# Kernel tuning notes

Hardware: AMD Instinct MI355X
Metric: run time of the kernel (lower is better)

The kernel has to match this reference:

```python
import jax, jax.numpy as jnp
import numpy as np

N, E, B, H, L = 50000, 800000, 256, 128, 4
AF, EF, GF, T = 108, 41, 239, 5
EPS = 1e-5


def _ln(x, g, b):
    m = jnp.mean(x, -1, keepdims=True)
    v = jnp.var(x, -1, keepdims=True)
    return (x - m) * jax.lax.rsqrt(v + EPS) * g + b


def setup_inputs() -> dict:
    key = jax.random.key(0)
    ks = jax.random.split(key, 20)
    w = lambda k, s: jax.random.normal(k, s, jnp.float32) * 0.05
    return {
        "x": jax.random.normal(ks[0], (N, AF), jnp.float32),
        "edge_attr": jax.random.normal(ks[1], (E, EF), jnp.float32),
        "global_features": jax.random.normal(ks[2], (B, GF), jnp.float32),
        "ae_w1": w(ks[3], (AF, H)), "ae_b1": jnp.zeros((H,), jnp.float32),
        "ae_w2": w(ks[4], (H, H)), "ae_b2": jnp.zeros((H,), jnp.float32),
        "ew1": w(ks[5], (L, EF, H)), "eb1": jnp.zeros((L, H), jnp.float32),
        "ew2": w(ks[6], (L, H, H)), "eb2": jnp.zeros((L, H), jnp.float32),
        "nw1": w(ks[7], (L, H, H)), "nb1": jnp.zeros((L, H), jnp.float32),
        "nw2": w(ks[8], (L, H, H)), "nb2": jnp.zeros((L, H), jnp.float32),
        "ln_g": jnp.ones((L, H), jnp.float32), "ln_b": jnp.zeros((L, H), jnp.float32),
        "gw": w(ks[9], (GF, H)), "gb": jnp.zeros((H,), jnp.float32),
        "ow1": w(ks[10], (2 * H, H)), "ob1": jnp.zeros((H,), jnp.float32),
        "ow2": w(ks[11], (H, H // 2)), "ob2": jnp.zeros((H // 2,), jnp.float32),
        "ow3": w(ks[12], (H // 2, T)), "ob3": jnp.zeros((T,), jnp.float32),
        "edge_index": jax.random.randint(ks[13], (2, E), 0, N, jnp.int32),
        "batch": jnp.sort(jax.random.randint(ks[14], (N,), 0, B, jnp.int32)),
    }


def reference(x, edge_attr, global_features, ae_w1, ae_b1, ae_w2, ae_b2,
              ew1, eb1, ew2, eb2, nw1, nb1, nw2, nb2, ln_g, ln_b,
              gw, gb, ow1, ob1, ow2, ob2, ow3, ob3, edge_index, batch):
    silu = jax.nn.silu
    # atom embedding
    h = silu(x @ ae_w1 + ae_b1) @ ae_w2 + ae_b2  # [N,H]
    src, dst = edge_index[0], edge_index[1]
    for l in range(L):
        # continuous-filter: edge MLP -> gather x_j -> multiply -> scatter-add
        Wf = silu(edge_attr @ ew1[l] + eb1[l]) @ ew2[l] + eb2[l]  # [E,H]
        msg = h[src] * Wf                                          # [E,H]
        agg = jax.ops.segment_sum(msg, dst, num_segments=N)        # [N,H]
        out = silu(agg @ nw1[l] + nb1[l]) @ nw2[l] + nb2[l]
        h = _ln(h + out, ln_g[l], ln_b[l])
    # global mean pool over graphs
    counts = jnp.clip(jax.ops.segment_sum(jnp.ones((N,), jnp.float32), batch, num_segments=B), 1.0)
    graph = jax.ops.segment_sum(h, batch, num_segments=B) / counts[:, None]  # [B,H]
    gp = silu(global_features @ gw + gb)                                      # [B,H]
    comb = jnp.concatenate([graph, gp], axis=-1)                              # [B,2H]
    hid = silu(silu(comb @ ow1 + ob1) @ ow2 + ob2)  # dropout is identity in eval
    return hid @ ow3 + ob3                           # [B,T]
```

## Files before the change

### kernel.cpp

```cpp
#include <hip/hip_runtime.h>
#include <math.h>

#define NATOM 50000
#define NEDGE 800000
#define NGRAPH 256
#define HD 128
#define NL 4
#define AFD 108
#define EFD 41
#define GFD 239
#define TOUT 5
#define LNEPS 1e-5f

typedef __attribute__((ext_vector_type(8))) short short8;
typedef __attribute__((ext_vector_type(4))) float f32x4;

__device__ __forceinline__ float silu_f(float v) {
    return v * __builtin_amdgcn_rcpf(1.f + __expf(-v));
}

__device__ __forceinline__ unsigned short f2b(float f) {
    union { float f; unsigned u; } x; x.f = f;
    unsigned r = x.u + 0x7fffu + ((x.u >> 16) & 1u);
    return (unsigned short)(r >> 16);
}

__global__ void hist_kernel(const int* __restrict__ dst, int* __restrict__ count) {
    for (int e = blockIdx.x * blockDim.x + threadIdx.x; e < NEDGE; e += gridDim.x * blockDim.x)
        atomicAdd(&count[dst[e]], 1);
}

__global__ void scan_kernel(const int* __restrict__ count, int* __restrict__ rowptr,
                            int* __restrict__ cursor) {
    __shared__ int s_w[4];
    __shared__ int s_carry;
    const int t = threadIdx.x, lane = t & 63, wv = t >> 6;
    if (t == 0) { s_carry = 0; rowptr[0] = 0; }
    __syncthreads();
    for (int base = 0; base < NATOM; base += 256) {
        int v = (base + t < NATOM) ? count[base + t] : 0;
        int x = v;
#pragma unroll
        for (int off = 1; off < 64; off <<= 1) {
            int y = __shfl_up(x, off);
            if (lane >= off) x += y;
        }
        if (lane == 63) s_w[wv] = x;
        __syncthreads();
        int wvoff = s_carry;
        for (int w = 0; w < wv; w++) wvoff += s_w[w];
        int incl = x + wvoff;
        if (base + t < NATOM) { rowptr[base + t + 1] = incl; cursor[base + t] = incl - v; }
        __syncthreads();
        if (t == 255) s_carry = incl;
        __syncthreads();
    }
}

__global__ void pos_kernel(const int* __restrict__ dst, const int* __restrict__ src,
                           int* __restrict__ cursor, int* __restrict__ pos,
                           int* __restrict__ ssrc) {
    for (int e = blockIdx.x * blockDim.x + threadIdx.x; e < NEDGE; e += gridDim.x * blockDim.x) {
        int d = dst[e];
        int p = atomicAdd(&cursor[d], 1);
        pos[e] = p;
        if (ssrc) ssrc[p] = src[e];
    }
}

__global__ void wconv_kernel(const float* __restrict__ ew1, const float* __restrict__ ew2,
                             unsigned short* __restrict__ w1t, unsigned short* __restrict__ w2t) {
    int idx = blockIdx.x * 256 + threadIdx.x;
    const int n1 = NL * HD * 64;
    if (idx < n1) {
        int l = idx / (HD * 64); int rem = idx - l * HD * 64; int n = rem >> 6; int k = rem & 63;
        float v = (k < EFD) ? ew1[((size_t)l * EFD + k) * HD + n] : 0.f;
        w1t[idx] = f2b(v);
    } else {
        int j = idx - n1;
        if (j < NL * HD * HD) {
            int l = j / (HD * HD); int rem = j - l * HD * HD; int n = rem >> 7; int k = rem & 127;
            w2t[j] = f2b(ew2[((size_t)l * HD + k) * HD + n]);
        }
    }
}

__global__ __launch_bounds__(256, 2) void atom_kernel(
    const float* __restrict__ x, const float* __restrict__ w1, const float* __restrict__ b1,
    const float* __restrict__ w2, const float* __restrict__ b2, float* __restrict__ h)
{
    __shared__ float s_x[64 * AFD];
    __shared__ float s_hid[64 * HD];
    const int t = threadIdx.x, cg = t & 31, rg = t >> 5, c4 = cg * 4;
    const int r0 = blockIdx.x * 64;

    for (int i = t; i < 64 * AFD; i += 256) {
        size_t g = (size_t)r0 * AFD + i;
        s_x[i] = (g < (size_t)NATOM * AFD) ? x[g] : 0.f;
    }
    float4 bb1 = *(const float4*)&b1[c4];
    float4 bb2 = *(const float4*)&b2[c4];
    __syncthreads();

    float4 acc[8];
#pragma unroll
    for (int i = 0; i < 8; i++) acc[i] = bb1;
    for (int k = 0; k < AFD; k++) {
        float4 w = *(const float4*)&w1[k * HD + c4];
#pragma unroll
        for (int i = 0; i < 8; i++) {
            float a = s_x[(rg * 8 + i) * AFD + k];
            acc[i].x += a * w.x; acc[i].y += a * w.y; acc[i].z += a * w.z; acc[i].w += a * w.w;
        }
    }
#pragma unroll
    for (int i = 0; i < 8; i++) {
        float4 v = acc[i];
        v.x = silu_f(v.x); v.y = silu_f(v.y); v.z = silu_f(v.z); v.w = silu_f(v.w);
        *(float4*)&s_hid[(rg * 8 + i) * HD + c4] = v;
    }
    __syncthreads();

    float4 o[8];
#pragma unroll
    for (int i = 0; i < 8; i++) o[i] = bb2;
    for (int j = 0; j < HD; j++) {
        float4 w = *(const float4*)&w2[j * HD + c4];
#pragma unroll
        for (int i = 0; i < 8; i++) {
            float a = s_hid[(rg * 8 + i) * HD + j];
            o[i].x += a * w.x; o[i].y += a * w.y; o[i].z += a * w.z; o[i].w += a * w.w;
        }
    }
#pragma unroll
    for (int i = 0; i < 8; i++) {
        int r = r0 + rg * 8 + i;
        if (r < NATOM) *(float4*)&h[(size_t)r * HD + c4] = o[i];
    }
}

__global__ __launch_bounds__(256) void wf_kernel(
    const float* __restrict__ edge_attr,
    const unsigned short* __restrict__ w1t, const float* __restrict__ b1,
    const unsigned short* __restrict__ w2t, const float* __restrict__ b2,
    const int* __restrict__ pos, float* __restrict__ wf)
{
    __shared__ __align__(16) unsigned short s_a1[64 * 64];
    __shared__ __align__(16) unsigned short s_hid[64 * 128];
    __shared__ __align__(16) float s_out[32 * 132];
    __shared__ int s_pos[64];

    const int t = threadIdx.x;
    const int wv = t >> 6, lane = t & 63;
    const int lr = lane & 15, lk = lane >> 4;

    short8 wb1[2][2], wb2[2][4];
    float b1v[2], b2v[2];
#pragma unroll
    for (int nt = 0; nt < 2; nt++) {
        int n = (wv * 2 + nt) * 16 + lr;
        b1v[nt] = b1[n]; b2v[nt] = b2[n];
#pragma unroll
        for (int kk = 0; kk < 2; kk++) wb1[nt][kk] = *(const short8*)&w1t[n * 64 + kk * 32 + lk * 8];
#pragma unroll
        for (int kk = 0; kk < 4; kk++) wb2[nt][kk] = *(const short8*)&w2t[n * 128 + kk * 32 + lk * 8];
    }

    int stg_byte[11];
    bool stg_ok[11];
#pragma unroll
    for (int j = 0; j < 11; j++) {
        int i = t + j * 256;
        stg_ok[j] = (i < 64 * EFD);
        int e = i / EFD, k = i - e * EFD;
        stg_byte[j] = e * 128 + ((2 * k) ^ ((e & 7) << 4));
    }

    for (int i = t; i < 64 * 64; i += 256) s_a1[i] = 0;
    __syncthreads();

    const int tc = t & 31, tr8 = t >> 5;
    const int ntiles = NEDGE / 64;
    for (int tile = blockIdx.x; tile < ntiles; tile += gridDim.x) {
        const int e0 = tile * 64;
        if (t < 64) s_pos[t] = pos[e0 + t];
        const float* ea = edge_attr + (size_t)e0 * EFD;
#pragma unroll
        for (int j = 0; j < 11; j++)
            if (stg_ok[j])
                *(unsigned short*)((char*)s_a1 + stg_byte[j]) = f2b(ea[t + j * 256]);
        __syncthreads();

        f32x4 acc1[4][2];
#pragma unroll
        for (int rt = 0; rt < 4; rt++) {
            int row = rt * 16 + lr;
            int sw = (row & 7) << 4;
            short8 a0 = *(const short8*)((const char*)s_a1 + row * 128 + ((lk * 16) ^ sw));
            short8 a1 = *(const short8*)((const char*)s_a1 + row * 128 + ((64 + lk * 16) ^ sw));
#pragma unroll
            for (int nt = 0; nt < 2; nt++) {
                f32x4 c = {0.f, 0.f, 0.f, 0.f};
                c = __builtin_amdgcn_mfma_f32_16x16x32_bf16(a0, wb1[nt][0], c, 0, 0, 0);
                c = __builtin_amdgcn_mfma_f32_16x16x32_bf16(a1, wb1[nt][1], c, 0, 0, 0);
                acc1[rt][nt] = c;
            }
        }
#pragma unroll
        for (int rt = 0; rt < 4; rt++) {
#pragma unroll
            for (int nt = 0; nt < 2; nt++) {
#pragma unroll
                for (int r = 0; r < 4; r++) {
                    int row = rt * 16 + lk * 4 + r;
                    int col = (wv * 2 + nt) * 16 + lr;
                    float v = silu_f(acc1[rt][nt][r] + b1v[nt]);
                    int byte = row * 256 + ((2 * col) ^ ((row & 7) << 4));
                    *(unsigned short*)((char*)s_hid + byte) = f2b(v);
                }
            }
        }
        __syncthreads();

        f32x4 acc2[4][2];
#pragma unroll
        for (int rt = 0; rt < 4; rt++) {
            int row = rt * 16 + lr;
            int sw = (row & 7) << 4;
            short8 ha[4];
#pragma unroll
            for (int kk = 0; kk < 4; kk++)
                ha[kk] = *(const short8*)((const char*)s_hid + row * 256 + ((kk * 64 + lk * 16) ^ sw));
#pragma unroll
            for (int nt = 0; nt < 2; nt++) {
                f32x4 c = {0.f, 0.f, 0.f, 0.f};
#pragma unroll
                for (int kk = 0; kk < 4; kk++)
                    c = __builtin_amdgcn_mfma_f32_16x16x32_bf16(ha[kk], wb2[nt][kk], c, 0, 0, 0);
                acc2[rt][nt] = c;
            }
        }

#pragma unroll
        for (int hf = 0; hf < 2; hf++) {
#pragma unroll
            for (int rr = 0; rr < 2; rr++) {
                int rt = hf * 2 + rr;
#pragma unroll
                for (int nt = 0; nt < 2; nt++)
#pragma unroll
                    for (int r = 0; r < 4; r++)
                        s_out[(rr * 16 + lk * 4 + r) * 132 + (wv * 2 + nt) * 16 + lr] =
                            silu_f(acc2[rt][nt][r] + b2v[nt]);
            }
            __syncthreads();
#pragma unroll
            for (int i = 0; i < 4; i++) {
                int lrow = tr8 * 4 + i;
                int p = s_pos[hf * 32 + lrow];
                *(float4*)&wf[(size_t)p * HD + tc * 4] = *(const float4*)&s_out[lrow * 132 + tc * 4];
            }
            __syncthreads();
        }
    }
}

__global__ void mul_kernel(const float* __restrict__ h, const int* __restrict__ src,
                           const int* __restrict__ pos, float* __restrict__ wf) {
    for (long long idx = (long long)blockIdx.x * 256 + threadIdx.x;
         idx < (long long)NEDGE * 32; idx += (long long)gridDim.x * 256) {
        int e = (int)(idx >> 5), q = (int)(idx & 31);
        int p = pos[e], s = src[e];
        float4 w = *(const float4*)&wf[(size_t)p * HD + q * 4];
        float4 hv = *(const float4*)&h[(size_t)s * HD + q * 4];
        w.x *= hv.x; w.y *= hv.y; w.z *= hv.z; w.w *= hv.w;
        *(float4*)&wf[(size_t)p * HD + q * 4] = w;
    }
}

template<bool GATHER>
__global__ __launch_bounds__(256, 2) void node_kernel(
    const float* __restrict__ wfm, const int* __restrict__ rowptr, const int* __restrict__ ssrc,
    const float* __restrict__ h_in,
    const float* __restrict__ w1, const float* __restrict__ b1,
    const float* __restrict__ w2, const float* __restrict__ b2,
    const float* __restrict__ lg, const float* __restrict__ lb,
    float* __restrict__ h_out)
{
    __shared__ float s_in[64 * HD];
    __shared__ float s_hid[64 * HD];
    __shared__ int s_rp[65];
    const int t = threadIdx.x, cg = t & 31, rg = t >> 5, c4 = cg * 4;
    const int r0 = blockIdx.x * 64;

    if (t < 65) {
        int idx = r0 + t;
        if (idx > NATOM) idx = NATOM;
        s_rp[t] = rowptr[idx];
    }
    float4 bb1 = *(const float4*)&b1[c4];
    float4 bb2 = *(const float4*)&b2[c4];
    float4 g4 = *(const float4*)&lg[c4];
    float4 lb4 = *(const float4*)&lb[c4];
    __syncthreads();

#pragma unroll
    for (int i = 0; i < 8; i++) {
        int rr = rg * 8 + i;
        int beg = s_rp[rr], end = s_rp[rr + 1];
        float4 a0 = make_float4(0.f, 0.f, 0.f, 0.f);
        float4 a1 = make_float4(0.f, 0.f, 0.f, 0.f);
        float4 a2 = make_float4(0.f, 0.f, 0.f, 0.f);
        float4 a3 = make_float4(0.f, 0.f, 0.f, 0.f);
        int p = beg;
        for (; p + 3 < end; p += 4) {
            float4 m0 = *(const float4*)&wfm[(size_t)(p + 0) * HD + c4];
            float4 m1 = *(const float4*)&wfm[(size_t)(p + 1) * HD + c4];
            float4 m2 = *(const float4*)&wfm[(size_t)(p + 2) * HD + c4];
            float4 m3 = *(const float4*)&wfm[(size_t)(p + 3) * HD + c4];
            if (GATHER) {
                int s0 = ssrc[p + 0], s1 = ssrc[p + 1], s2 = ssrc[p + 2], s3 = ssrc[p + 3];
                float4 h0 = *(const float4*)&h_in[(size_t)s0 * HD + c4];
                float4 h1 = *(const float4*)&h_in[(size_t)s1 * HD + c4];
                float4 h2 = *(const float4*)&h_in[(size_t)s2 * HD + c4];
                float4 h3 = *(const float4*)&h_in[(size_t)s3 * HD + c4];
                a0.x = fmaf(m0.x, h0.x, a0.x); a0.y = fmaf(m0.y, h0.y, a0.y);
                a0.z = fmaf(m0.z, h0.z, a0.z); a0.w = fmaf(m0.w, h0.w, a0.w);
                a1.x = fmaf(m1.x, h1.x, a1.x); a1.y = fmaf(m1.y, h1.y, a1.y);
                a1.z = fmaf(m1.z, h1.z, a1.z); a1.w = fmaf(m1.w, h1.w, a1.w);
                a2.x = fmaf(m2.x, h2.x, a2.x); a2.y = fmaf(m2.y, h2.y, a2.y);
                a2.z = fmaf(m2.z, h2.z, a2.z); a2.w = fmaf(m2.w, h2.w, a2.w);
                a3.x = fmaf(m3.x, h3.x, a3.x); a3.y = fmaf(m3.y, h3.y, a3.y);
                a3.z = fmaf(m3.z, h3.z, a3.z); a3.w = fmaf(m3.w, h3.w, a3.w);
            } else {
                a0.x += m0.x; a0.y += m0.y; a0.z += m0.z; a0.w += m0.w;
                a1.x += m1.x; a1.y += m1.y; a1.z += m1.z; a1.w += m1.w;
                a2.x += m2.x; a2.y += m2.y; a2.z += m2.z; a2.w += m2.w;
                a3.x += m3.x; a3.y += m3.y; a3.z += m3.z; a3.w += m3.w;
            }
        }
        for (; p < end; p++) {
            float4 m0 = *(const float4*)&wfm[(size_t)p * HD + c4];
            if (GATHER) {
                int s0 = ssrc[p];
                float4 h0 = *(const float4*)&h_in[(size_t)s0 * HD + c4];
                a0.x = fmaf(m0.x, h0.x, a0.x); a0.y = fmaf(m0.y, h0.y, a0.y);
                a0.z = fmaf(m0.z, h0.z, a0.z); a0.w = fmaf(m0.w, h0.w, a0.w);
            } else {
                a0.x += m0.x; a0.y += m0.y; a0.z += m0.z; a0.w += m0.w;
            }
        }
        a0.x += a1.x + a2.x + a3.x; a0.y += a1.y + a2.y + a3.y;
        a0.z += a1.z + a2.z + a3.z; a0.w += a1.w + a2.w + a3.w;
        *(float4*)&s_in[rr * HD + c4] = a0;
    }
    __syncthreads();

    float4 acc[8];
#pragma unroll
    for (int i = 0; i < 8; i++) acc[i] = bb1;
    for (int k = 0; k < HD; k++) {
        float4 w = *(const float4*)&w1[k * HD + c4];
#pragma unroll
        for (int i = 0; i < 8; i++) {
            float a = s_in[(rg * 8 + i) * HD + k];
            acc[i].x += a * w.x; acc[i].y += a * w.y; acc[i].z += a * w.z; acc[i].w += a * w.w;
        }
    }
#pragma unroll
    for (int i = 0; i < 8; i++) {
        float4 v = acc[i];
        v.x = silu_f(v.x); v.y = silu_f(v.y); v.z = silu_f(v.z); v.w = silu_f(v.w);
        *(float4*)&s_hid[(rg * 8 + i) * HD + c4] = v;
    }
    __syncthreads();

    float4 o[8];
#pragma unroll
    for (int i = 0; i < 8; i++) o[i] = bb2;
    for (int j = 0; j < HD; j++) {
        float4 w = *(const float4*)&w2[j * HD + c4];
#pragma unroll
        for (int i = 0; i < 8; i++) {
            float a = s_hid[(rg * 8 + i) * HD + j];
            o[i].x += a * w.x; o[i].y += a * w.y; o[i].z += a * w.z; o[i].w += a * w.w;
        }
    }
#pragma unroll
    for (int i = 0; i < 8; i++) {
        int r = r0 + rg * 8 + i;
        float4 hv = make_float4(0.f, 0.f, 0.f, 0.f);
        if (r < NATOM) hv = *(const float4*)&h_in[(size_t)r * HD + c4];
        float4 v;
        v.x = hv.x + o[i].x; v.y = hv.y + o[i].y; v.z = hv.z + o[i].z; v.w = hv.w + o[i].w;
        float s1 = v.x + v.y + v.z + v.w;
        float s2 = v.x * v.x + v.y * v.y + v.z * v.z + v.w * v.w;
#pragma unroll
        for (int off = 16; off >= 1; off >>= 1) {
            s1 += __shfl_xor(s1, off);
            s2 += __shfl_xor(s2, off);
        }
        float mean = s1 * (1.f / HD);
        float var = s2 * (1.f / HD) - mean * mean;
        float rstd = rsqrtf(var + LNEPS);
        float4 y;
        y.x = (v.x - mean) * rstd * g4.x + lb4.x;
        y.y = (v.y - mean) * rstd * g4.y + lb4.y;
        y.z = (v.z - mean) * rstd * g4.z + lb4.z;
        y.w = (v.w - mean) * rstd * g4.w + lb4.w;
        if (r < NATOM) *(float4*)&h_out[(size_t)r * HD + c4] = y;
    }
}

__global__ __launch_bounds__(128) void head_kernel(
    const float* __restrict__ h, const float* __restrict__ gfeat,
    const float* __restrict__ gw, const float* __restrict__ gb,
    const float* __restrict__ ow1, const float* __restrict__ ob1,
    const float* __restrict__ ow2, const float* __restrict__ ob2,
    const float* __restrict__ ow3, const float* __restrict__ ob3,
    const int* __restrict__ batch, float* __restrict__ out)
{
    __shared__ float comb[2 * HD];
    __shared__ float h1[HD];
    __shared__ float h2[64];
    const int b = blockIdx.x;
    const int c = threadIdx.x;

    int lo = 0, hi = NATOM;
    while (lo < hi) { int m = (lo + hi) >> 1; if (batch[m] < b) lo = m + 1; else hi = m; }
    const int start = lo;
    hi = NATOM;
    while (lo < hi) { int m = (lo + hi) >> 1; if (batch[m] < b + 1) lo = m + 1; else hi = m; }
    const int end = lo;

    float s = 0.f;
    for (int r = start; r < end; r++) s += h[(size_t)r * HD + c];
    float cnt = (float)(end - start);
    if (cnt < 1.f) cnt = 1.f;
    comb[c] = s / cnt;

    float a = gb[c];
    for (int k = 0; k < GFD; k++) a += gfeat[b * GFD + k] * gw[k * HD + c];
    comb[HD + c] = silu_f(a);
    __syncthreads();

    float u = ob1[c];
    for (int j = 0; j < 2 * HD; j++) u += comb[j] * ow1[j * HD + c];
    h1[c] = silu_f(u);
    __syncthreads();

    if (c < 64) {
        float v = ob2[c];
        for (int j = 0; j < HD; j++) v += h1[j] * ow2[j * 64 + c];
        h2[c] = silu_f(v);
    }
    __syncthreads();

    if (c < TOUT) {
        float v = ob3[c];
        for (int j = 0; j < 64; j++) v += h2[j] * ow3[j * TOUT + c];
        out[b * TOUT + c] = v;
    }
}

extern "C" void kernel_launch(void* const* d_in, const int* in_sizes, int n_in,
                              void* d_out, int out_size, void* d_ws, size_t ws_size,
                              hipStream_t stream) {
    const float* x        = (const float*)d_in[0];
    const float* edge_attr= (const float*)d_in[1];
    const float* gfeat    = (const float*)d_in[2];
    const float* ae_w1    = (const float*)d_in[3];
    const float* ae_b1    = (const float*)d_in[4];
    const float* ae_w2    = (const float*)d_in[5];
    const float* ae_b2    = (const float*)d_in[6];
    const float* ew1      = (const float*)d_in[7];
    const float* eb1      = (const float*)d_in[8];
    const float* ew2      = (const float*)d_in[9];
    const float* eb2      = (const float*)d_in[10];
    const float* nw1      = (const float*)d_in[11];
    const float* nb1      = (const float*)d_in[12];
    const float* nw2      = (const float*)d_in[13];
    const float* nb2      = (const float*)d_in[14];
    const float* ln_g     = (const float*)d_in[15];
    const float* ln_b     = (const float*)d_in[16];
    const float* gw       = (const float*)d_in[17];
    const float* gb       = (const float*)d_in[18];
    const float* ow1      = (const float*)d_in[19];
    const float* ob1      = (const float*)d_in[20];
    const float* ow2      = (const float*)d_in[21];
    const float* ob2      = (const float*)d_in[22];
    const float* ow3      = (const float*)d_in[23];
    const float* ob3      = (const float*)d_in[24];
    const int* edge_index = (const int*)d_in[25];
    const int* batch      = (const int*)d_in[26];

    const int* src = edge_index;
    const int* dst = edge_index + NEDGE;
    const int row_blocks = (NATOM + 63) / 64;

    float* h0 = (float*)d_ws;
    size_t fA = (size_t)NATOM * HD * 2 + (size_t)NEDGE * HD;
    size_t intsA = (size_t)NATOM * 3 + 4 + (size_t)NEDGE * 2;
    size_t wele = (size_t)NL * HD * 64 + (size_t)NL * HD * HD;
    size_t needA = fA * 4 + intsA * 4 + wele * 2;

    bool modeA = (ws_size >= needA);

    float* h1   = modeA ? (h0 + (size_t)NATOM * HD) : h0;
    float* wf   = (modeA ? h1 : h0) + (size_t)NATOM * HD;
    int* count  = (int*)(wf + (size_t)NEDGE * HD);
    int* rowptr = count + NATOM;
    int* cursor = rowptr + NATOM + 4;
    int* pos    = cursor + NATOM;
    int* ssrc   = modeA ? (pos + NEDGE) : nullptr;
    unsigned short* w1t = (unsigned short*)(modeA ? (ssrc + NEDGE) : (pos + NEDGE));
    unsigned short* w2t = w1t + NL * HD * 64;

    hipMemsetAsync(count, 0, NATOM * sizeof(int), stream);
    hist_kernel<<<1024, 256, 0, stream>>>(dst, count);
    scan_kernel<<<1, 256, 0, stream>>>(count, rowptr, cursor);
    pos_kernel<<<1024, 256, 0, stream>>>(dst, src, cursor, pos, ssrc);
    wconv_kernel<<<(NL * HD * 64 + NL * HD * HD + 255) / 256, 256, 0, stream>>>(ew1, ew2, w1t, w2t);

    atom_kernel<<<row_blocks, 256, 0, stream>>>(x, ae_w1, ae_b1, ae_w2, ae_b2, h0);

    const float* cur = h0;
    float* nxt = modeA ? h1 : h0;
    for (int l = 0; l < NL; l++) {
        wf_kernel<<<2048, 256, 0, stream>>>(
            edge_attr,
            w1t + (size_t)l * HD * 64, eb1 + (size_t)l * HD,
            w2t + (size_t)l * HD * HD, eb2 + (size_t)l * HD,
            pos, wf);
        if (modeA) {
            node_kernel<true><<<row_blocks, 256, 0, stream>>>(
                wf, rowptr, ssrc, cur,
                nw1 + (size_t)l * HD * HD, nb1 + (size_t)l * HD,
                nw2 + (size_t)l * HD * HD, nb2 + (size_t)l * HD,
                ln_g + (size_t)l * HD, ln_b + (size_t)l * HD,
                nxt);
            const float* tmp = cur; cur = nxt; nxt = (float*)tmp;
        } else {
            mul_kernel<<<2048, 256, 0, stream>>>(h0, src, pos, wf);
            node_kernel<false><<<row_blocks, 256, 0, stream>>>(
                wf, rowptr, nullptr, h0,
                nw1 + (size_t)l * HD * HD, nb1 + (size_t)l * HD,
                nw2 + (size_t)l * HD * HD, nb2 + (size_t)l * HD,
                ln_g + (size_t)l * HD, ln_b + (size_t)l * HD,
                h0);
        }
    }

    head_kernel<<<NGRAPH, 128, 0, stream>>>(
        cur, gfeat, gw, gb, ow1, ob1, ow2, ob2, ow3, ob3, batch, (float*)d_out);
}
```

Measured before the change: 2.208 ms.

## Widen scan, shrink LDS in wf and node kernels, unroll pooling sum

```diff
diff --git a/kernel.cpp b/kernel.cpp
--- a/kernel.cpp
+++ b/kernel.cpp
@@ -32,12 +32,12 @@
 
 __global__ void scan_kernel(const int* __restrict__ count, int* __restrict__ rowptr,
                             int* __restrict__ cursor) {
-    __shared__ int s_w[4];
+    __shared__ int s_w[16];
     __shared__ int s_carry;
     const int t = threadIdx.x, lane = t & 63, wv = t >> 6;
     if (t == 0) { s_carry = 0; rowptr[0] = 0; }
     __syncthreads();
-    for (int base = 0; base < NATOM; base += 256) {
+    for (int base = 0; base < NATOM; base += 1024) {
         int v = (base + t < NATOM) ? count[base + t] : 0;
         int x = v;
 #pragma unroll
@@ -52,7 +52,7 @@
         int incl = x + wvoff;
         if (base + t < NATOM) { rowptr[base + t + 1] = incl; cursor[base + t] = incl - v; }
         __syncthreads();
-        if (t == 255) s_carry = incl;
+        if (t == 1023) s_carry = incl;
         __syncthreads();
     }
 }
@@ -147,7 +147,7 @@
 {
     __shared__ __align__(16) unsigned short s_a1[64 * 64];
     __shared__ __align__(16) unsigned short s_hid[64 * 128];
-    __shared__ __align__(16) float s_out[32 * 132];
+    __shared__ __align__(16) float s_out[16 * 132];
     __shared__ int s_pos[64];
 
     const int t = threadIdx.x;
@@ -242,22 +242,18 @@
         }
 
 #pragma unroll
-        for (int hf = 0; hf < 2; hf++) {
-#pragma unroll
-            for (int rr = 0; rr < 2; rr++) {
-                int rt = hf * 2 + rr;
-#pragma unroll
-                for (int nt = 0; nt < 2; nt++)
-#pragma unroll
-                    for (int r = 0; r < 4; r++)
-                        s_out[(rr * 16 + lk * 4 + r) * 132 + (wv * 2 + nt) * 16 + lr] =
-                            silu_f(acc2[rt][nt][r] + b2v[nt]);
-            }
+        for (int hf = 0; hf < 4; hf++) {
+#pragma unroll
+            for (int nt = 0; nt < 2; nt++)
+#pragma unroll
+                for (int r = 0; r < 4; r++)
+                    s_out[(lk * 4 + r) * 132 + (wv * 2 + nt) * 16 + lr] =
+                        silu_f(acc2[hf][nt][r] + b2v[nt]);
             __syncthreads();
 #pragma unroll
-            for (int i = 0; i < 4; i++) {
-                int lrow = tr8 * 4 + i;
-                int p = s_pos[hf * 32 + lrow];
+            for (int i = 0; i < 2; i++) {
+                int lrow = tr8 * 2 + i;
+                int p = s_pos[hf * 16 + lrow];
                 *(float4*)&wf[(size_t)p * HD + tc * 4] = *(const float4*)&s_out[lrow * 132 + tc * 4];
             }
             __syncthreads();
@@ -279,7 +275,7 @@
 }
 
 template<bool GATHER>
-__global__ __launch_bounds__(256, 2) void node_kernel(
+__global__ __launch_bounds__(256) void node_kernel(
     const float* __restrict__ wfm, const int* __restrict__ rowptr, const int* __restrict__ ssrc,
     const float* __restrict__ h_in,
     const float* __restrict__ w1, const float* __restrict__ b1,
@@ -287,8 +283,7 @@
     const float* __restrict__ lg, const float* __restrict__ lb,
     float* __restrict__ h_out)
 {
-    __shared__ float s_in[64 * HD];
-    __shared__ float s_hid[64 * HD];
+    __shared__ float s_buf[64 * HD];
     __shared__ int s_rp[65];
     const int t = threadIdx.x, cg = t & 31, rg = t >> 5, c4 = cg * 4;
     const int r0 = blockIdx.x * 64;
@@ -352,7 +347,7 @@
         }
         a0.x += a1.x + a2.x + a3.x; a0.y += a1.y + a2.y + a3.y;
         a0.z += a1.z + a2.z + a3.z; a0.w += a1.w + a2.w + a3.w;
-        *(float4*)&s_in[rr * HD + c4] = a0;
+        *(float4*)&s_buf[rr * HD + c4] = a0;
     }
     __syncthreads();
 
@@ -363,15 +358,16 @@
         float4 w = *(const float4*)&w1[k * HD + c4];
 #pragma unroll
         for (int i = 0; i < 8; i++) {
-            float a = s_in[(rg * 8 + i) * HD + k];
+            float a = s_buf[(rg * 8 + i) * HD + k];
             acc[i].x += a * w.x; acc[i].y += a * w.y; acc[i].z += a * w.z; acc[i].w += a * w.w;
         }
     }
+    __syncthreads();
 #pragma unroll
     for (int i = 0; i < 8; i++) {
         float4 v = acc[i];
         v.x = silu_f(v.x); v.y = silu_f(v.y); v.z = silu_f(v.z); v.w = silu_f(v.w);
-        *(float4*)&s_hid[(rg * 8 + i) * HD + c4] = v;
+        *(float4*)&s_buf[(rg * 8 + i) * HD + c4] = v;
     }
     __syncthreads();
 
@@ -382,7 +378,7 @@
         float4 w = *(const float4*)&w2[j * HD + c4];
 #pragma unroll
         for (int i = 0; i < 8; i++) {
-            float a = s_hid[(rg * 8 + i) * HD + j];
+            float a = s_buf[(rg * 8 + i) * HD + j];
             o[i].x += a * w.x; o[i].y += a * w.y; o[i].z += a * w.z; o[i].w += a * w.w;
         }
     }
@@ -433,8 +429,16 @@
     while (lo < hi) { int m = (lo + hi) >> 1; if (batch[m] < b + 1) lo = m + 1; else hi = m; }
     const int end = lo;
 
-    float s = 0.f;
-    for (int r = start; r < end; r++) s += h[(size_t)r * HD + c];
+    float s0 = 0.f, s1 = 0.f, s2 = 0.f, s3 = 0.f;
+    int r = start;
+    for (; r + 3 < end; r += 4) {
+        s0 += h[(size_t)(r + 0) * HD + c];
+        s1 += h[(size_t)(r + 1) * HD + c];
+        s2 += h[(size_t)(r + 2) * HD + c];
+        s3 += h[(size_t)(r + 3) * HD + c];
+    }
+    for (; r < end; r++) s0 += h[(size_t)r * HD + c];
+    float s = (s0 + s1) + (s2 + s3);
     float cnt = (float)(end - start);
     if (cnt < 1.f) cnt = 1.f;
     comb[c] = s / cnt;
@@ -518,7 +522,7 @@
 
     hipMemsetAsync(count, 0, NATOM * sizeof(int), stream);
     hist_kernel<<<1024, 256, 0, stream>>>(dst, count);
-    scan_kernel<<<1, 256, 0, stream>>>(count, rowptr, cursor);
+    scan_kernel<<<1, 1024, 0, stream>>>(count, rowptr, cursor);
     pos_kernel<<<1024, 256, 0, stream>>>(dst, src, cursor, pos, ssrc);
     wconv_kernel<<<(NL * HD * 64 + NL * HD * HD + 255) / 256, 256, 0, stream>>>(ew1, ew2, w1t, w2t);
 
```

After: 1.994 ms. 1.11x faster.
